# Kernel tuning notes

Measured on AMD Instinct MI355X. Metric: run time of the kernel, lower is better.

## Reference

```python
import jax, jax.numpy as jnp
import numpy as np

MAX_LENGTH = 10
SOS = 0
H = 1024
V = 32000
B = 256
S = 64


def setup_inputs() -> dict:
    key = jax.random.key(0)
    ks = jax.random.split(key, 16)
    sc = 1.0 / np.sqrt(H)
    return {
        "encoder_outputs": jax.random.normal(ks[0], (B, S, H), jnp.float32),
        "encoder_hidden": jax.random.normal(ks[1], (1, B, H), jnp.float32),
        "target_tensor": jax.random.randint(ks[2], (B, MAX_LENGTH), 0, V),
        "embedding": jax.random.normal(ks[3], (V, H), jnp.float32),
        "Wa_w": jax.random.uniform(ks[4], (H, H), jnp.float32, -sc, sc),
        "Wa_b": jax.random.uniform(ks[5], (H,), jnp.float32, -sc, sc),
        "Ua_w": jax.random.uniform(ks[6], (H, H), jnp.float32, -sc, sc),
        "Ua_b": jax.random.uniform(ks[7], (H,), jnp.float32, -sc, sc),
        "Va_w": jax.random.uniform(ks[8], (1, H), jnp.float32, -sc, sc),
        "Va_b": jax.random.uniform(ks[9], (1,), jnp.float32, -sc, sc),
        "gru_w_ih": jax.random.uniform(ks[10], (3 * H, 2 * H), jnp.float32, -sc, sc),
        "gru_w_hh": jax.random.uniform(ks[11], (3 * H, H), jnp.float32, -sc, sc),
        "gru_b_ih": jax.random.uniform(ks[12], (3 * H,), jnp.float32, -sc, sc),
        "gru_b_hh": jax.random.uniform(ks[13], (3 * H,), jnp.float32, -sc, sc),
        "out_w": jax.random.uniform(ks[14], (V, H), jnp.float32, -sc, sc),
        "out_b": jax.random.uniform(ks[15], (V,), jnp.float32, -sc, sc),
    }


def reference(encoder_outputs, encoder_hidden, target_tensor, embedding,
              Wa_w, Wa_b, Ua_w, Ua_b, Va_w, Va_b,
              gru_w_ih, gru_w_hh, gru_b_ih, gru_b_hh, out_w, out_b):
    keys = encoder_outputs                      # [B,S,H]
    # Ua(keys) is step-invariant: hoist out of the decode loop.
    Uk = jnp.einsum('bsh,kh->bsk', keys, Ua_w) + Ua_b  # [B,S,H]
    h0 = encoder_hidden[0]                      # [B,H]
    # teacher forcing: input at step i is SOS for i=0 else target[:, i-1]
    toks = jnp.concatenate(
        [jnp.full((B, 1), SOS, dtype=target_tensor.dtype),
         target_tensor[:, :MAX_LENGTH - 1]], axis=1).T  # [T,B]

    def step(h, tok):
        emb = embedding[tok]                               # [B,H] (dropout = identity in eval)
        wq = jnp.dot(h, Wa_w.T) + Wa_b                     # [B,H]
        e = jnp.tanh(wq[:, None, :] + Uk)                  # [B,S,H]
        scores = jnp.einsum('bsh,h->bs', e, Va_w[0]) + Va_b[0]
        w = jax.nn.softmax(scores, axis=-1)                # [B,S]
        ctx = jnp.einsum('bs,bsh->bh', w, keys)            # [B,H]
        x = jnp.concatenate([emb, ctx], axis=-1)           # [B,2H]
        gi = jnp.dot(x, gru_w_ih.T) + gru_b_ih             # [B,3H]
        gh = jnp.dot(h, gru_w_hh.T) + gru_b_hh             # [B,3H]
        ir, iz, inn = jnp.split(gi, 3, axis=-1)
        hr, hz, hn = jnp.split(gh, 3, axis=-1)
        r = jax.nn.sigmoid(ir + hr)
        z = jax.nn.sigmoid(iz + hz)
        n = jnp.tanh(inn + r * hn)
        h2 = (1.0 - z) * n + z * h                         # [B,H]
        logits = jnp.dot(h2, out_w.T) + out_b              # [B,V]
        return h2, (logits, w)

    h_last, (logits, attn) = jax.lax.scan(step, h0, toks)
    dec_out = jax.nn.log_softmax(jnp.transpose(logits, (1, 0, 2)), axis=-1)  # [B,T,V]
    attentions = jnp.transpose(attn, (1, 0, 2))            # [B,T,S]
    return dec_out, h_last[None, :, :], attentions
```

## Files before the change

### kernel.cpp

```cpp
#include <hip/hip_runtime.h>
#include <math.h>

#define H 1024
#define V 32000
#define B 256
#define S 64
#define T 10

#define GBK 32

typedef __attribute__((ext_vector_type(8))) short bf16x8;
typedef __attribute__((ext_vector_type(4))) float f32x4;

static __device__ __forceinline__ unsigned short f2bf(float f) {
  unsigned int u = __float_as_uint(f);
  u += 0x7fff + ((u >> 16) & 1);
  return (unsigned short)(u >> 16);
}
static __device__ __forceinline__ float bf2f(unsigned short u) {
  return __uint_as_float(((unsigned int)u) << 16);
}
static __device__ __forceinline__ float fast_tanh(float x) {
  float e = __expf(2.f * x);
  return 1.f - 2.f * __builtin_amdgcn_rcpf(e + 1.f);
}
static __device__ __forceinline__ float fast_sigmoid(float x) {
  return __builtin_amdgcn_rcpf(1.f + __expf(-x));
}

static __device__ __forceinline__ void load_lds16(const void* g, void* l) {
  __builtin_amdgcn_global_load_lds(
      (const __attribute__((address_space(1))) unsigned int*)g,
      (__attribute__((address_space(3))) unsigned int*)l, 16, 0, 0);
}

static __device__ __forceinline__ int lds_off(int row, int g) {
  return row * GBK + ((g ^ ((row >> 1) & 3)) * 8);
}

template <int TM, int TN, int MODE, int GRIDMODE, int STAGES>
__global__ __launch_bounds__(256) void gemm_mfma(
    const unsigned short* __restrict__ A, const unsigned short* __restrict__ W,
    const float* __restrict__ aux, float* __restrict__ C,
    unsigned short* __restrict__ Cb, float* __restrict__ partials,
    int M, int N, int K, int ldc, int pstride) {
  constexpr int FM = TM / 32;
  constexpr int FN = TN / 32;
  constexpr int CA = TM / 64;
  constexpr int CB = TN / 64;
  constexpr int LOADS = CA + CB;
  constexpr int F = (STAGES >= 3) ? (STAGES - 2) : 0;

  __shared__ unsigned short lsA[STAGES][TM * GBK];
  __shared__ unsigned short lsB[STAGES][TN * GBK];
  const int tid = threadIdx.x;
  const int lane = tid & 63;
  const int w = tid >> 6;

  int mIdx, nIdx;
  if constexpr (GRIDMODE == 1) {
    const int nwg = gridDim.x * gridDim.y;
    const int orig = blockIdx.y * gridDim.x + blockIdx.x;
    const int q = nwg >> 3, rr = nwg & 7;
    const int xcd = orig & 7, rest = orig >> 3;
    const int wgid =
        (xcd < rr ? xcd * (q + 1) : rr * (q + 1) + (xcd - rr) * q) + rest;
    mIdx = wgid % gridDim.x;
    nIdx = wgid / gridDim.x;
  } else {
    mIdx = blockIdx.y;
    nIdx = blockIdx.x;
  }
  const int mBase = mIdx * TM;
  const int nBase = nIdx * TN;
  const int rowBase = (w >> 1) * (TM / 2);
  const int colBase = (w & 1) * (TN / 2);

  const int fr = lane & 15;
  const int fkU = lane >> 4;
  const int fg = lane >> 4;

  f32x4 acc[FM][FN] = {};

  auto STAGE = [&](int buf, int k0) {
#pragma unroll
    for (int i = 0; i < CA; ++i) {
      int chunk = i * 256 + tid;
      int row = chunk >> 2;
      int u = chunk & 3;
      int col = (u ^ ((row >> 1) & 3)) * 8;
      load_lds16(A + (size_t)(mBase + row) * K + k0 + col,
                 &lsA[buf][chunk * 8]);
    }
#pragma unroll
    for (int i = 0; i < CB; ++i) {
      int chunk = i * 256 + tid;
      int row = chunk >> 2;
      int u = chunk & 3;
      int col = (u ^ ((row >> 1) & 3)) * 8;
      load_lds16(W + (size_t)(nBase + row) * K + k0 + col,
                 &lsB[buf][chunk * 8]);
    }
  };

  const int NT = K / GBK;
  for (int s = 0; s <= F && s < NT; ++s) STAGE(s % STAGES, s * GBK);

  for (int t = 0; t < NT; ++t) {
    const int rem = NT - 1 - t;
    if (rem >= F) {
      asm volatile("s_waitcnt vmcnt(%0)\n\ts_barrier" :: "i"(F * LOADS)
                   : "memory");
    } else if (rem == 2) {
      asm volatile("s_waitcnt vmcnt(%0)\n\ts_barrier" :: "i"(2 * LOADS)
                   : "memory");
    } else if (rem == 1) {
      asm volatile("s_waitcnt vmcnt(%0)\n\ts_barrier" :: "i"(1 * LOADS)
                   : "memory");
    } else {
      asm volatile("s_waitcnt vmcnt(0)\n\ts_barrier" ::: "memory");
    }
    if (t + F + 1 < NT) STAGE((t + F + 1) % STAGES, (t + F + 1) * GBK);

    const int cb = t % STAGES;
    bf16x8 af[FM], bfr[FN];
#pragma unroll
    for (int m = 0; m < FM; ++m)
      af[m] = *(const bf16x8*)&lsA[cb][lds_off(rowBase + m * 16 + fr, fkU)];
#pragma unroll
    for (int n = 0; n < FN; ++n)
      bfr[n] = *(const bf16x8*)&lsB[cb][lds_off(colBase + n * 16 + fr, fkU)];
#pragma unroll
    for (int m = 0; m < FM; ++m)
#pragma unroll
      for (int n = 0; n < FN; ++n)
        acc[m][n] = __builtin_amdgcn_mfma_f32_16x16x32_bf16(
            af[m], bfr[n], acc[m][n], 0, 0, 0);
  }

#pragma unroll
  for (int m = 0; m < FM; ++m) {
    int colg[FN];
    float bv[FN];
#pragma unroll
    for (int n = 0; n < FN; ++n) {
      colg[n] = nBase + colBase + n * 16 + fr;
      if constexpr (MODE != 2) bv[n] = aux[colg[n]];
    }
#pragma unroll
    for (int r = 0; r < 4; ++r) {
      const int rowg = mBase + rowBase + m * 16 + fg * 4 + r;
      float v[FN];
#pragma unroll
      for (int n = 0; n < FN; ++n) {
        if constexpr (MODE == 2)
          v[n] = acc[m][n][r] + aux[(size_t)rowg * ldc + colg[n]];
        else
          v[n] = acc[m][n][r] + bv[n];
        if constexpr (MODE == 1 || MODE == 3)
          Cb[(size_t)rowg * ldc + colg[n]] = f2bf(v[n]);
        else
          C[(size_t)rowg * ldc + colg[n]] = v[n];
      }
      if constexpr (MODE == 3) {
        float mx = fmaxf(fmaxf(v[0], v[1]), fmaxf(v[2], v[3]));
        mx = fmaxf(mx, __shfl_xor(mx, 1, 64));
        mx = fmaxf(mx, __shfl_xor(mx, 2, 64));
        mx = fmaxf(mx, __shfl_xor(mx, 4, 64));
        mx = fmaxf(mx, __shfl_xor(mx, 8, 64));
        float se = __expf(v[0] - mx) + __expf(v[1] - mx) +
                   __expf(v[2] - mx) + __expf(v[3] - mx);
        se += __shfl_xor(se, 1, 64);
        se += __shfl_xor(se, 2, 64);
        se += __shfl_xor(se, 4, 64);
        se += __shfl_xor(se, 8, 64);
        if (fr == 0) {
          float2* pp = (float2*)partials;
          pp[(size_t)rowg * pstride + nIdx * 2 + (w & 1)] =
              make_float2(mx, se);
        }
      }
    }
  }
}

__global__ __launch_bounds__(256) void cvt_bf16_kernel(
    const float* __restrict__ src, unsigned short* __restrict__ dst) {
  size_t i = ((size_t)blockIdx.x * 256 + threadIdx.x) * 8;
  float4 a = *(const float4*)&src[i];
  float4 b = *(const float4*)&src[i + 4];
  ushort4 lo, hi;
  lo.x = f2bf(a.x); lo.y = f2bf(a.y); lo.z = f2bf(a.z); lo.w = f2bf(a.w);
  hi.x = f2bf(b.x); hi.y = f2bf(b.y); hi.z = f2bf(b.z); hi.w = f2bf(b.w);
  *(ushort4*)&dst[i] = lo;
  *(ushort4*)&dst[i + 4] = hi;
}

__global__ __launch_bounds__(256) void cvt_split_wih(
    const float* __restrict__ w_ih, unsigned short* __restrict__ Wemb,
    unsigned short* __restrict__ Wctx) {
  size_t base = ((size_t)blockIdx.x * 256 + threadIdx.x) * 8;
  int row = (int)(base >> 11);
  int col = (int)(base & 2047);
  float4 a = *(const float4*)&w_ih[base];
  float4 b = *(const float4*)&w_ih[base + 4];
  ushort4 lo, hi;
  lo.x = f2bf(a.x); lo.y = f2bf(a.y); lo.z = f2bf(a.z); lo.w = f2bf(a.w);
  hi.x = f2bf(b.x); hi.y = f2bf(b.y); hi.z = f2bf(b.z); hi.w = f2bf(b.w);
  unsigned short* dst = (col < H) ? (Wemb + (size_t)row * H + col)
                                  : (Wctx + (size_t)row * H + col - H);
  *(ushort4*)dst = lo;
  *(ushort4*)(dst + 4) = hi;
}

__global__ __launch_bounds__(256) void build_fused_bias(
    const float* __restrict__ Wa_b, const float* __restrict__ b_hh,
    float* __restrict__ fb) {
  int i = blockIdx.x * 256 + threadIdx.x;
  fb[i] = (i < H) ? Wa_b[i] : b_hh[i - H];
}

__global__ __launch_bounds__(256) void embed_all_kernel(
    const int* __restrict__ target, const float* __restrict__ emb,
    unsigned short* __restrict__ embAll) {
  int idx = blockIdx.x * 256 + threadIdx.x;
  int h8 = (idx & 127) * 8;
  int tb = idx >> 7;
  int t = tb >> 8;
  int b = tb & 255;
  int tok = (t == 0) ? 0 : target[b * T + (t - 1)];
  const float* e = emb + (size_t)tok * H + h8;
  float4 a = *(const float4*)e;
  float4 c = *(const float4*)(e + 4);
  ushort4 lo, hi;
  lo.x = f2bf(a.x); lo.y = f2bf(a.y); lo.z = f2bf(a.z); lo.w = f2bf(a.w);
  hi.x = f2bf(c.x); hi.y = f2bf(c.y); hi.z = f2bf(c.z); hi.w = f2bf(c.w);
  unsigned short* d = embAll + (size_t)tb * H + h8;
  *(ushort4*)d = lo;
  *(ushort4*)(d + 4) = hi;
}

__global__ __launch_bounds__(256) void attn_fused_kernel(
    const float* __restrict__ wqgh, const unsigned short* __restrict__ Uk_bf,
    const unsigned short* __restrict__ keys_bf,
    const float* __restrict__ Va_w, const float* __restrict__ Va_b,
    float* __restrict__ out_attn, unsigned short* __restrict__ ctx_bf, int t) {
  const int b = blockIdx.x;
  const int tid = threadIdx.x;
  __shared__ float wqs[H];
  __shared__ float vas[H];
  __shared__ float sw[S];

  ((float4*)wqs)[tid] = ((const float4*)(wqgh + (size_t)b * 4 * H))[tid];
  ((float4*)vas)[tid] = ((const float4*)Va_w)[tid];
  __syncthreads();

  const int s = tid >> 2;
  const int hc = (tid & 3) * 256;
  const unsigned short* uk = Uk_bf + ((size_t)b * S + s) * H + hc;
  float sum = 0.f;
#pragma unroll 4
  for (int i = 0; i < 256; i += 8) {
    bf16x8 u = *(const bf16x8*)&uk[i];
#pragma unroll
    for (int j = 0; j < 8; ++j) {
      float e = fast_tanh(wqs[hc + i + j] + bf2f((unsigned short)u[j]));
      sum += e * vas[hc + i + j];
    }
  }
  sum += __shfl_xor(sum, 1, 64);
  sum += __shfl_xor(sum, 2, 64);
  if ((tid & 3) == 0) sw[s] = sum + Va_b[0];
  __syncthreads();

  if (tid < 64) {
    float v = sw[tid];
    float m = v;
    for (int off = 32; off > 0; off >>= 1) m = fmaxf(m, __shfl_xor(m, off, 64));
    float e = __expf(v - m);
    float sm = e;
    for (int off = 32; off > 0; off >>= 1) sm += __shfl_xor(sm, off, 64);
    float wv = e / sm;
    sw[tid] = wv;
    out_attn[((size_t)b * T + t) * S + tid] = wv;
  }
  __syncthreads();

  const unsigned short* kb = keys_bf + (size_t)b * S * H + tid * 4;
  float c0 = 0.f, c1 = 0.f, c2 = 0.f, c3 = 0.f;
#pragma unroll 8
  for (int s2 = 0; s2 < S; ++s2) {
    float wv = sw[s2];
    ushort4 kv = *(const ushort4*)&kb[(size_t)s2 * H];
    c0 += wv * bf2f(kv.x);
    c1 += wv * bf2f(kv.y);
    c2 += wv * bf2f(kv.z);
    c3 += wv * bf2f(kv.w);
  }
  ushort4 o;
  o.x = f2bf(c0); o.y = f2bf(c1); o.z = f2bf(c2); o.w = f2bf(c3);
  *(ushort4*)&ctx_bf[(size_t)b * H + tid * 4] = o;
}

__global__ __launch_bounds__(256) void gru_kernel(
    const float* __restrict__ gi, const float* __restrict__ wqgh,
    const float* __restrict__ h_in, float* __restrict__ h_out,
    unsigned short* __restrict__ h_out_bf) {
  int idx = blockIdx.x * 256 + threadIdx.x;
  int b = idx >> 10;
  int j = idx & (H - 1);
  const float* gib = gi + (size_t)b * 3 * H;
  const float* ghb = wqgh + (size_t)b * 4 * H + H;
  float r = fast_sigmoid(gib[j] + ghb[j]);
  float z = fast_sigmoid(gib[H + j] + ghb[H + j]);
  float n = fast_tanh(gib[2 * H + j] + r * ghb[2 * H + j]);
  float hp = h_in[idx];
  float ho = (1.f - z) * n + z * hp;
  h_out[idx] = ho;
  h_out_bf[idx] = f2bf(ho);
}

__global__ __launch_bounds__(256) void logsm_reduce_kernel(
    const float* __restrict__ partials, float* __restrict__ ls, int P) {
  const int row = blockIdx.x;
  const int tid = threadIdx.x;
  const float2* pp = (const float2*)partials + (size_t)row * P;
  __shared__ float red[256];
  float mx = -INFINITY;
  for (int i = tid; i < P; i += 256) mx = fmaxf(mx, pp[i].x);
  red[tid] = mx;
  __syncthreads();
  for (int off = 128; off > 0; off >>= 1) {
    if (tid < off) red[tid] = fmaxf(red[tid], red[tid + off]);
    __syncthreads();
  }
  mx = red[0];
  __syncthreads();
  float sm = 0.f;
  for (int i = tid; i < P; i += 256) sm += pp[i].y * __expf(pp[i].x - mx);
  red[tid] = sm;
  __syncthreads();
  for (int off = 128; off > 0; off >>= 1) {
    if (tid < off) red[tid] += red[tid + off];
    __syncthreads();
  }
  if (tid == 0) ls[row] = mx + __logf(red[0]);
}

__global__ __launch_bounds__(256) void logsm_sub_kernel(
    const unsigned short* __restrict__ logits_bf, const float* __restrict__ ls,
    float* __restrict__ dec) {
  const int tb = blockIdx.y;
  const int t = tb >> 8;
  const int b = tb & 255;
  const int i8 = (blockIdx.x * 256 + threadIdx.x) * 8;
  if (i8 < V) {
    float l = ls[tb];
    const unsigned short* src = logits_bf + (size_t)tb * V + i8;
    bf16x8 u = *(const bf16x8*)src;
    float* d = dec + (size_t)b * T * V + (size_t)t * V + i8;
    float4 o0, o1;
    o0.x = bf2f((unsigned short)u[0]) - l; o0.y = bf2f((unsigned short)u[1]) - l;
    o0.z = bf2f((unsigned short)u[2]) - l; o0.w = bf2f((unsigned short)u[3]) - l;
    o1.x = bf2f((unsigned short)u[4]) - l; o1.y = bf2f((unsigned short)u[5]) - l;
    o1.z = bf2f((unsigned short)u[6]) - l; o1.w = bf2f((unsigned short)u[7]) - l;
    *(float4*)d = o0;
    *(float4*)(d + 4) = o1;
  }
}

__global__ __launch_bounds__(256) void copy_kernel(
    const float* __restrict__ src, float* __restrict__ dst, int n) {
  int i = blockIdx.x * 256 + threadIdx.x;
  if (i < n) dst[i] = src[i];
}

extern "C" void kernel_launch(void* const* d_in, const int* in_sizes, int n_in,
                              void* d_out, int out_size, void* d_ws, size_t ws_size,
                              hipStream_t stream) {
  const float* keys       = (const float*)d_in[0];
  const float* enc_hidden = (const float*)d_in[1];
  const int*   target     = (const int*)d_in[2];
  const float* embedding  = (const float*)d_in[3];
  const float* Wa_w = (const float*)d_in[4];
  const float* Wa_b = (const float*)d_in[5];
  const float* Ua_w = (const float*)d_in[6];
  const float* Ua_b = (const float*)d_in[7];
  const float* Va_w = (const float*)d_in[8];
  const float* Va_b = (const float*)d_in[9];
  const float* gru_w_ih = (const float*)d_in[10];
  const float* gru_w_hh = (const float*)d_in[11];
  const float* gru_b_ih = (const float*)d_in[12];
  const float* gru_b_hh = (const float*)d_in[13];
  const float* out_w = (const float*)d_in[14];
  const float* out_b = (const float*)d_in[15];

  float* out = (float*)d_out;
  float* out_dec  = out;
  float* out_h    = out + (size_t)B * T * V;
  float* out_attn = out + (size_t)B * T * V + (size_t)B * H;

  char* p = (char*)d_ws;
  unsigned short* keys_bf = (unsigned short*)p; p += (size_t)B * S * H * 2;
  unsigned short* outw_bf = (unsigned short*)p; p += (size_t)V * H * 2;
  unsigned short* Uaw_bf  = (unsigned short*)p; p += (size_t)H * H * 2;
  unsigned short* fusedW  = (unsigned short*)p; p += (size_t)4 * H * H * 2;
  float*          fusedB  = (float*)p;          p += (size_t)4 * H * 4;
  unsigned short* Wemb_bf = (unsigned short*)p; p += (size_t)3 * H * H * 2;
  unsigned short* Wctx_bf = (unsigned short*)p; p += (size_t)3 * H * H * 2;
  unsigned short* embAll  = (unsigned short*)p; p += (size_t)T * B * H * 2;
  unsigned short* Uk_bf   = (unsigned short*)p; p += (size_t)B * S * H * 2;
  float*          giE     = (float*)p;          p += (size_t)T * B * 3 * H * 4;
  float*          wqgh    = (float*)p;          p += (size_t)B * 4 * H * 4;
  unsigned short* ctx_bf  = (unsigned short*)p; p += (size_t)B * H * 2;
  float*          gi      = (float*)p;          p += (size_t)B * 3 * H * 4;
  float*          hA      = (float*)p;          p += (size_t)B * H * 4;
  float*          hB      = (float*)p;          p += (size_t)B * H * 4;
  unsigned short* hAll    = (unsigned short*)p; p += (size_t)(T + 1) * B * H * 2;
  unsigned short* logits_bf = (unsigned short*)p; p += (size_t)T * B * V * 2;
  float*          parts   = (float*)p;          p += (size_t)T * B * 500 * 2 * 4;
  float*          ls      = (float*)p;          p += (size_t)T * B * 4;

  cvt_bf16_kernel<<<(B * S * H) / 2048, 256, 0, stream>>>(keys, keys_bf);
  cvt_bf16_kernel<<<((size_t)V * H) / 2048, 256, 0, stream>>>(out_w, outw_bf);
  cvt_bf16_kernel<<<(H * H) / 2048, 256, 0, stream>>>(Ua_w, Uaw_bf);
  cvt_bf16_kernel<<<(H * H) / 2048, 256, 0, stream>>>(Wa_w, fusedW);
  cvt_bf16_kernel<<<(3 * H * H) / 2048, 256, 0, stream>>>(gru_w_hh,
                                                          fusedW + (size_t)H * H);
  build_fused_bias<<<(4 * H) / 256, 256, 0, stream>>>(Wa_b, gru_b_hh, fusedB);
  cvt_split_wih<<<(3 * H * 2 * H) / 2048, 256, 0, stream>>>(gru_w_ih, Wemb_bf,
                                                            Wctx_bf);
  embed_all_kernel<<<(T * B * H / 8) / 256, 256, 0, stream>>>(target, embedding,
                                                              embAll);
  cvt_bf16_kernel<<<(B * H) / 2048, 256, 0, stream>>>(enc_hidden, hAll);

  gemm_mfma<128, 128, 1, 0, 2>
      <<<dim3(H / 128, (B * S) / 128), 256, 0, stream>>>(
          keys_bf, Uaw_bf, Ua_b, nullptr, Uk_bf, nullptr, B * S, H, H, H, 0);
  gemm_mfma<128, 128, 0, 1, 2>
      <<<dim3((T * B) / 128, 3 * H / 128), 256, 0, stream>>>(
          embAll, Wemb_bf, gru_b_ih, giE, nullptr, nullptr, T * B, 3 * H, H,
          3 * H, 0);

  const float* h_in = enc_hidden;
  float* hbufs[2] = {hA, hB};

  for (int t = 0; t < T; ++t) {
    const unsigned short* hbf_in = hAll + (size_t)t * B * H;
    unsigned short* hbf_out = hAll + (size_t)(t + 1) * B * H;
    float* h_out = hbufs[t & 1];

    gemm_mfma<64, 64, 0, 1, 5><<<dim3(B / 64, 4 * H / 64), 256, 0, stream>>>(
        hbf_in, fusedW, fusedB, wqgh, nullptr, nullptr, B, 4 * H, H, 4 * H, 0);
    attn_fused_kernel<<<B, 256, 0, stream>>>(
        wqgh, Uk_bf, keys_bf, Va_w, Va_b, out_attn, ctx_bf, t);
    gemm_mfma<64, 64, 2, 1, 5><<<dim3(B / 64, 3 * H / 64), 256, 0, stream>>>(
        ctx_bf, Wctx_bf, giE + (size_t)t * B * 3 * H, gi, nullptr, nullptr,
        B, 3 * H, H, 3 * H, 0);
    gru_kernel<<<(B * H) / 256, 256, 0, stream>>>(gi, wqgh, h_in, h_out,
                                                  hbf_out);

    h_in = h_out;
  }

  gemm_mfma<64, 128, 3, 1, 2>
      <<<dim3((T * B) / 64, V / 128), 256, 0, stream>>>(
          hAll + (size_t)B * H, outw_bf, out_b, nullptr, logits_bf, parts,
          T * B, V, H, V, 500);
  logsm_reduce_kernel<<<T * B, 256, 0, stream>>>(parts, ls, 500);
  logsm_sub_kernel<<<dim3((V + 2047) / 2048, T * B), 256, 0, stream>>>(
      logits_bf, ls, out_dec);

  copy_kernel<<<(B * H + 255) / 256, 256, 0, stream>>>(h_in, out_h, B * H);
}
```

Measured before the change: 1.076 ms.

## Compute output logits GEMM in FP8 with new 128x128 MFMA kernel

The final vocabulary projection now uses FP8 weights and FP8 hidden states, computed by a dedicated FP8 MFMA kernel with 128x128 tiles and a double-buffered, swizzled LDS. The GRU kernel is vectorised to four elements per thread and also writes an FP8 copy of the hidden state. The output weight is converted to FP8 instead of bf16. The aim is to halve the bytes and double the MFMA throughput of the largest GEMM, at the cost of lower numeric precision in the logits.

```diff
diff --git a/kernel.cpp b/kernel.cpp
--- a/kernel.cpp
+++ b/kernel.cpp
@@ -42,8 +42,8 @@
 __global__ __launch_bounds__(256) void gemm_mfma(
     const unsigned short* __restrict__ A, const unsigned short* __restrict__ W,
     const float* __restrict__ aux, float* __restrict__ C,
-    unsigned short* __restrict__ Cb, float* __restrict__ partials,
-    int M, int N, int K, int ldc, int pstride) {
+    unsigned short* __restrict__ Cb,
+    int M, int N, int K, int ldc) {
   constexpr int FM = TM / 32;
   constexpr int FN = TN / 32;
   constexpr int CA = TM / 64;
@@ -157,28 +157,128 @@
           v[n] = acc[m][n][r] + aux[(size_t)rowg * ldc + colg[n]];
         else
           v[n] = acc[m][n][r] + bv[n];
-        if constexpr (MODE == 1 || MODE == 3)
+        if constexpr (MODE == 1)
           Cb[(size_t)rowg * ldc + colg[n]] = f2bf(v[n]);
         else
           C[(size_t)rowg * ldc + colg[n]] = v[n];
       }
-      if constexpr (MODE == 3) {
-        float mx = fmaxf(fmaxf(v[0], v[1]), fmaxf(v[2], v[3]));
-        mx = fmaxf(mx, __shfl_xor(mx, 1, 64));
-        mx = fmaxf(mx, __shfl_xor(mx, 2, 64));
-        mx = fmaxf(mx, __shfl_xor(mx, 4, 64));
-        mx = fmaxf(mx, __shfl_xor(mx, 8, 64));
-        float se = __expf(v[0] - mx) + __expf(v[1] - mx) +
-                   __expf(v[2] - mx) + __expf(v[3] - mx);
-        se += __shfl_xor(se, 1, 64);
-        se += __shfl_xor(se, 2, 64);
-        se += __shfl_xor(se, 4, 64);
-        se += __shfl_xor(se, 8, 64);
-        if (fr == 0) {
-          float2* pp = (float2*)partials;
-          pp[(size_t)rowg * pstride + nIdx * 2 + (w & 1)] =
-              make_float2(mx, se);
-        }
+    }
+  }
+}
+
+__global__ __launch_bounds__(256) void gemm_fp8_logits(
+    const unsigned char* __restrict__ A8, const unsigned char* __restrict__ W8,
+    const float* __restrict__ bias, unsigned short* __restrict__ Cb,
+    float* __restrict__ partials, int M, int N, int K, int ldc, int pstride) {
+  constexpr int BK = 64;
+  __shared__ __align__(16) unsigned char lsA[2][128 * BK];
+  __shared__ __align__(16) unsigned char lsB[2][128 * BK];
+  const int tid = threadIdx.x;
+  const int lane = tid & 63;
+  const int w = tid >> 6;
+
+  const int nwg = gridDim.x * gridDim.y;
+  const int orig = blockIdx.y * gridDim.x + blockIdx.x;
+  const int q = nwg >> 3, rr = nwg & 7;
+  const int xcd = orig & 7, rest = orig >> 3;
+  const int wgid =
+      (xcd < rr ? xcd * (q + 1) : rr * (q + 1) + (xcd - rr) * q) + rest;
+  const int mIdx = wgid % gridDim.x;
+  const int nIdx = wgid / gridDim.x;
+  const int mBase = mIdx * 128;
+  const int nBase = nIdx * 128;
+  const int rowBase = (w >> 1) * 64;
+  const int colBase = (w & 1) * 64;
+  const int fr = lane & 15;
+  const int fkU = lane >> 4;
+  const int fg = lane >> 4;
+
+  f32x4 acc[4][4] = {};
+
+  auto STAGE = [&](int buf, int k0) {
+#pragma unroll
+    for (int i = 0; i < 2; ++i) {
+      int c = i * 256 + tid;
+      int row = c >> 2;
+      int u = c & 3;
+      int col = (u ^ (row & 3)) * 16;
+      load_lds16(A8 + (size_t)(mBase + row) * K + k0 + col, &lsA[buf][c * 16]);
+    }
+#pragma unroll
+    for (int i = 0; i < 2; ++i) {
+      int c = i * 256 + tid;
+      int row = c >> 2;
+      int u = c & 3;
+      int col = (u ^ (row & 3)) * 16;
+      load_lds16(W8 + (size_t)(nBase + row) * K + k0 + col, &lsB[buf][c * 16]);
+    }
+  };
+
+  const int NT = K / BK;
+  STAGE(0, 0);
+  int cb = 0;
+  for (int t = 0; t < NT; ++t) {
+    asm volatile("s_waitcnt vmcnt(0)\n\ts_barrier" ::: "memory");
+    if (t + 1 < NT) STAGE(cb ^ 1, (t + 1) * BK);
+#pragma unroll
+    for (int ks = 0; ks < 2; ++ks) {
+      const int u = ks * 2 + (fkU >> 1);
+      const int sub = (fkU & 1) * 8;
+      long long af[4], bf[4];
+#pragma unroll
+      for (int m = 0; m < 4; ++m) {
+        int row = rowBase + m * 16 + fr;
+        af[m] = *(const long long*)
+            &lsA[cb][row * BK + ((u ^ (row & 3)) << 4) + sub];
+      }
+#pragma unroll
+      for (int n = 0; n < 4; ++n) {
+        int row = colBase + n * 16 + fr;
+        bf[n] = *(const long long*)
+            &lsB[cb][row * BK + ((u ^ (row & 3)) << 4) + sub];
+      }
+#pragma unroll
+      for (int m = 0; m < 4; ++m)
+#pragma unroll
+        for (int n = 0; n < 4; ++n)
+          acc[m][n] = __builtin_amdgcn_mfma_f32_16x16x32_fp8_fp8(
+              af[m], bf[n], acc[m][n], 0, 0, 0);
+    }
+    cb ^= 1;
+  }
+
+#pragma unroll
+  for (int m = 0; m < 4; ++m) {
+    int colg[4];
+    float bv[4];
+#pragma unroll
+    for (int n = 0; n < 4; ++n) {
+      colg[n] = nBase + colBase + n * 16 + fr;
+      bv[n] = bias[colg[n]];
+    }
+#pragma unroll
+    for (int r = 0; r < 4; ++r) {
+      const int rowg = mBase + rowBase + m * 16 + fg * 4 + r;
+      float v[4];
+#pragma unroll
+      for (int n = 0; n < 4; ++n) {
+        v[n] = acc[m][n][r] + bv[n];
+        Cb[(size_t)rowg * ldc + colg[n]] = f2bf(v[n]);
+      }
+      float mx = fmaxf(fmaxf(v[0], v[1]), fmaxf(v[2], v[3]));
+      mx = fmaxf(mx, __shfl_xor(mx, 1, 64));
+      mx = fmaxf(mx, __shfl_xor(mx, 2, 64));
+      mx = fmaxf(mx, __shfl_xor(mx, 4, 64));
+      mx = fmaxf(mx, __shfl_xor(mx, 8, 64));
+      float se = __expf(v[0] - mx) + __expf(v[1] - mx) +
+                 __expf(v[2] - mx) + __expf(v[3] - mx);
+      se += __shfl_xor(se, 1, 64);
+      se += __shfl_xor(se, 2, 64);
+      se += __shfl_xor(se, 4, 64);
+      se += __shfl_xor(se, 8, 64);
+      if (fr == 0) {
+        float2* pp = (float2*)partials;
+        pp[(size_t)rowg * pstride + nIdx * 2 + (w & 1)] = make_float2(mx, se);
       }
     }
   }
@@ -194,6 +294,18 @@
   hi.x = f2bf(b.x); hi.y = f2bf(b.y); hi.z = f2bf(b.z); hi.w = f2bf(b.w);
   *(ushort4*)&dst[i] = lo;
   *(ushort4*)&dst[i + 4] = hi;
+}
+
+__global__ __launch_bounds__(256) void cvt_fp8_kernel(
+    const float* __restrict__ src, unsigned int* __restrict__ dst) {
+  size_t i = (size_t)blockIdx.x * 256 + threadIdx.x;
+  float4 a = ((const float4*)src)[i * 2];
+  float4 b = ((const float4*)src)[i * 2 + 1];
+  int lo = __builtin_amdgcn_cvt_pk_fp8_f32(a.x, a.y, 0, false);
+  lo = __builtin_amdgcn_cvt_pk_fp8_f32(a.z, a.w, lo, true);
+  int hi = __builtin_amdgcn_cvt_pk_fp8_f32(b.x, b.y, 0, false);
+  hi = __builtin_amdgcn_cvt_pk_fp8_f32(b.z, b.w, hi, true);
+  ((int2*)dst)[i] = make_int2(lo, hi);
 }
 
 __global__ __launch_bounds__(256) void cvt_split_wih(
@@ -305,19 +417,46 @@
 __global__ __launch_bounds__(256) void gru_kernel(
     const float* __restrict__ gi, const float* __restrict__ wqgh,
     const float* __restrict__ h_in, float* __restrict__ h_out,
-    unsigned short* __restrict__ h_out_bf) {
-  int idx = blockIdx.x * 256 + threadIdx.x;
+    unsigned short* __restrict__ h_out_bf, unsigned int* __restrict__ h_out_f8) {
+  int idx = (blockIdx.x * 256 + threadIdx.x) * 4;
   int b = idx >> 10;
   int j = idx & (H - 1);
   const float* gib = gi + (size_t)b * 3 * H;
   const float* ghb = wqgh + (size_t)b * 4 * H + H;
-  float r = fast_sigmoid(gib[j] + ghb[j]);
-  float z = fast_sigmoid(gib[H + j] + ghb[H + j]);
-  float n = fast_tanh(gib[2 * H + j] + r * ghb[2 * H + j]);
-  float hp = h_in[idx];
-  float ho = (1.f - z) * n + z * hp;
-  h_out[idx] = ho;
-  h_out_bf[idx] = f2bf(ho);
+  float4 gr4 = *(const float4*)&gib[j];
+  float4 gz4 = *(const float4*)&gib[H + j];
+  float4 gn4 = *(const float4*)&gib[2 * H + j];
+  float4 hr4 = *(const float4*)&ghb[j];
+  float4 hz4 = *(const float4*)&ghb[H + j];
+  float4 hn4 = *(const float4*)&ghb[2 * H + j];
+  float4 hp4 = *(const float4*)&h_in[idx];
+  float4 ho4;
+  {
+    float r0 = fast_sigmoid(gr4.x + hr4.x);
+    float z0 = fast_sigmoid(gz4.x + hz4.x);
+    float n0 = fast_tanh(gn4.x + r0 * hn4.x);
+    ho4.x = (1.f - z0) * n0 + z0 * hp4.x;
+    float r1 = fast_sigmoid(gr4.y + hr4.y);
+    float z1 = fast_sigmoid(gz4.y + hz4.y);
+    float n1 = fast_tanh(gn4.y + r1 * hn4.y);
+    ho4.y = (1.f - z1) * n1 + z1 * hp4.y;
+    float r2 = fast_sigmoid(gr4.z + hr4.z);
+    float z2 = fast_sigmoid(gz4.z + hz4.z);
+    float n2 = fast_tanh(gn4.z + r2 * hn4.z);
+    ho4.z = (1.f - z2) * n2 + z2 * hp4.z;
+    float r3 = fast_sigmoid(gr4.w + hr4.w);
+    float z3 = fast_sigmoid(gz4.w + hz4.w);
+    float n3 = fast_tanh(gn4.w + r3 * hn4.w);
+    ho4.w = (1.f - z3) * n3 + z3 * hp4.w;
+  }
+  ushort4 hb4;
+  hb4.x = f2bf(ho4.x); hb4.y = f2bf(ho4.y);
+  hb4.z = f2bf(ho4.z); hb4.w = f2bf(ho4.w);
+  int p8 = __builtin_amdgcn_cvt_pk_fp8_f32(ho4.x, ho4.y, 0, false);
+  p8 = __builtin_amdgcn_cvt_pk_fp8_f32(ho4.z, ho4.w, p8, true);
+  *(float4*)&h_out[idx] = ho4;
+  *(ushort4*)&h_out_bf[idx] = hb4;
+  h_out_f8[idx >> 2] = (unsigned int)p8;
 }
 
 __global__ __launch_bounds__(256) void logsm_reduce_kernel(
@@ -402,7 +541,7 @@
 
   char* p = (char*)d_ws;
   unsigned short* keys_bf = (unsigned short*)p; p += (size_t)B * S * H * 2;
-  unsigned short* outw_bf = (unsigned short*)p; p += (size_t)V * H * 2;
+  unsigned char*  outw8   = (unsigned char*)p;  p += (size_t)V * H;
   unsigned short* Uaw_bf  = (unsigned short*)p; p += (size_t)H * H * 2;
   unsigned short* fusedW  = (unsigned short*)p; p += (size_t)4 * H * H * 2;
   float*          fusedB  = (float*)p;          p += (size_t)4 * H * 4;
@@ -417,12 +556,14 @@
   float*          hA      = (float*)p;          p += (size_t)B * H * 4;
   float*          hB      = (float*)p;          p += (size_t)B * H * 4;
   unsigned short* hAll    = (unsigned short*)p; p += (size_t)(T + 1) * B * H * 2;
+  unsigned char*  hAll8   = (unsigned char*)p;  p += (size_t)T * B * H;
   unsigned short* logits_bf = (unsigned short*)p; p += (size_t)T * B * V * 2;
   float*          parts   = (float*)p;          p += (size_t)T * B * 500 * 2 * 4;
   float*          ls      = (float*)p;          p += (size_t)T * B * 4;
 
   cvt_bf16_kernel<<<(B * S * H) / 2048, 256, 0, stream>>>(keys, keys_bf);
-  cvt_bf16_kernel<<<((size_t)V * H) / 2048, 256, 0, stream>>>(out_w, outw_bf);
+  cvt_fp8_kernel<<<((size_t)V * H) / 2048, 256, 0, stream>>>(
+      out_w, (unsigned int*)outw8);
   cvt_bf16_kernel<<<(H * H) / 2048, 256, 0, stream>>>(Ua_w, Uaw_bf);
   cvt_bf16_kernel<<<(H * H) / 2048, 256, 0, stream>>>(Wa_w, fusedW);
   cvt_bf16_kernel<<<(3 * H * H) / 2048, 256, 0, stream>>>(gru_w_hh,
@@ -436,11 +577,10 @@
 
   gemm_mfma<128, 128, 1, 0, 2>
       <<<dim3(H / 128, (B * S) / 128), 256, 0, stream>>>(
-          keys_bf, Uaw_bf, Ua_b, nullptr, Uk_bf, nullptr, B * S, H, H, H, 0);
+          keys_bf, Uaw_bf, Ua_b, nullptr, Uk_bf, B * S, H, H, H);
   gemm_mfma<128, 128, 0, 1, 2>
       <<<dim3((T * B) / 128, 3 * H / 128), 256, 0, stream>>>(
-          embAll, Wemb_bf, gru_b_ih, giE, nullptr, nullptr, T * B, 3 * H, H,
-          3 * H, 0);
+          embAll, Wemb_bf, gru_b_ih, giE, nullptr, T * B, 3 * H, H, 3 * H);
 
   const float* h_in = enc_hidden;
   float* hbufs[2] = {hA, hB};
@@ -448,25 +588,24 @@
   for (int t = 0; t < T; ++t) {
     const unsigned short* hbf_in = hAll + (size_t)t * B * H;
     unsigned short* hbf_out = hAll + (size_t)(t + 1) * B * H;
+    unsigned int* h8_out = (unsigned int*)(hAll8 + (size_t)t * B * H);
     float* h_out = hbufs[t & 1];
 
     gemm_mfma<64, 64, 0, 1, 5><<<dim3(B / 64, 4 * H / 64), 256, 0, stream>>>(
-        hbf_in, fusedW, fusedB, wqgh, nullptr, nullptr, B, 4 * H, H, 4 * H, 0);
+        hbf_in, fusedW, fusedB, wqgh, nullptr, B, 4 * H, H, 4 * H);
     attn_fused_kernel<<<B, 256, 0, stream>>>(
         wqgh, Uk_bf, keys_bf, Va_w, Va_b, out_attn, ctx_bf, t);
     gemm_mfma<64, 64, 2, 1, 5><<<dim3(B / 64, 3 * H / 64), 256, 0, stream>>>(
-        ctx_bf, Wctx_bf, giE + (size_t)t * B * 3 * H, gi, nullptr, nullptr,
-        B, 3 * H, H, 3 * H, 0);
-    gru_kernel<<<(B * H) / 256, 256, 0, stream>>>(gi, wqgh, h_in, h_out,
-                                                  hbf_out);
+        ctx_bf, Wctx_bf, giE + (size_t)t * B * 3 * H, gi, nullptr,
+        B, 3 * H, H, 3 * H);
+    gru_kernel<<<(B * H / 4) / 256, 256, 0, stream>>>(gi, wqgh, h_in, h_out,
+                                                      hbf_out, h8_out);
 
     h_in = h_out;
   }
 
-  gemm_mfma<64, 128, 3, 1, 2>
-      <<<dim3((T * B) / 64, V / 128), 256, 0, stream>>>(
-          hAll + (size_t)B * H, outw_bf, out_b, nullptr, logits_bf, parts,
-          T * B, V, H, V, 500);
+  gemm_fp8_logits<<<dim3((T * B) / 128, V / 128), 256, 0, stream>>>(
+      hAll8, outw8, out_b, logits_bf, parts, T * B, V, H, V, 500);
   logsm_reduce_kernel<<<T * B, 256, 0, stream>>>(parts, ls, 500);
   logsm_sub_kernel<<<dim3((V + 2047) / 2048, T * B), 256, 0, stream>>>(
       logits_bf, ls, out_dec);
```

After: 981.4 us. 8.8% less time.
